# Kernel optimization log

Measured on AMD Instinct MI355X. Metric: run time of the kernel, lower is better.

Reference implementation:

```python
import jax, jax.numpy as jnp
import numpy as np

B, S, E = 1, 2048, 1024
H, KVH = 16, 8
D = E // H            # 64
N_REP = H // KVH      # 2
CLAMP = 50000.0
ROPE_BASE = 10000.0


def setup_inputs() -> dict:
    key = jax.random.key(0)
    ks = jax.random.split(key, 9)
    # RoPE tables: freqs_cis[t, i] = exp(1j * t * base^(-2i/D)), split into cos/sin
    inv_freq = 1.0 / (ROPE_BASE ** (jnp.arange(0, D, 2, dtype=jnp.float32) / D))  # [D/2]
    angles = jnp.arange(S, dtype=jnp.float32)[:, None] * inv_freq[None, :]        # [S, D/2]
    return {
        "x": jax.random.normal(ks[0], (B, S, E), jnp.float32),
        "attn_bias": jax.random.normal(ks[1], (B, H, S, S), jnp.float32) * 0.1,
        "freqs_cos": jnp.cos(angles),
        "freqs_sin": jnp.sin(angles),
        "wq_w": jax.random.normal(ks[2], (E, E), jnp.float32) * (E ** -0.5),
        "wk_w": jax.random.normal(ks[3], (KVH * D, E), jnp.float32) * (E ** -0.5),
        "wk_b": jax.random.normal(ks[4], (KVH * D,), jnp.float32) * 0.01,
        "wv_w": jax.random.normal(ks[5], (KVH * D, E), jnp.float32) * (E ** -0.5),
        "wv_b": jax.random.normal(ks[6], (KVH * D,), jnp.float32) * 0.01,
        "wo_w": jax.random.normal(ks[7], (E, E), jnp.float32) * (E ** -0.5),
        "wo_b": jax.random.normal(ks[8], (E,), jnp.float32) * 0.01,
    }


def _rope(t, cos, sin):
    # t: [b, s, h, d]; pairs (t[..., 2i], t[..., 2i+1]) treated as complex.
    tr = t.reshape(*t.shape[:-1], -1, 2)          # [b, s, h, d/2, 2]
    xr, xi = tr[..., 0], tr[..., 1]
    c = cos[None, :, None, :]                     # [1, s, 1, d/2]
    s = sin[None, :, None, :]
    out = jnp.stack([xr * c - xi * s, xr * s + xi * c], axis=-1)
    return out.reshape(t.shape)


def reference(x, attn_bias, freqs_cos, freqs_sin,
              wq_w, wk_w, wk_b, wv_w, wv_b, wo_w, wo_b):
    bsz, seqlen, _ = x.shape
    xq = (x @ wq_w.T).reshape(bsz, seqlen, H, D)
    xk = (x @ wk_w.T + wk_b).reshape(bsz, seqlen, KVH, D)
    xv = (x @ wv_w.T + wv_b).reshape(bsz, seqlen, KVH, D)
    # inline RoPE on q and k
    xq = _rope(xq, freqs_cos, freqs_sin)
    xk = _rope(xk, freqs_cos, freqs_sin)
    # GQA: repeat kv heads (kv-head h maps to query heads [h*n_rep, (h+1)*n_rep))
    keys = jnp.repeat(xk, N_REP, axis=2)          # [b, s, H, d]
    values = jnp.repeat(xv, N_REP, axis=2)
    # [b, h, q, k] scores with scaling, clamp, bias
    scores = jnp.einsum('bqhd,bkhd->bhqk', xq, keys) / jnp.sqrt(jnp.float32(D))
    scores = jnp.clip(scores, -CLAMP, CLAMP) + attn_bias
    attn_weights = jax.nn.softmax(scores.astype(jnp.float32), axis=-1).astype(xq.dtype)
    out = jnp.einsum('bhqk,bkhd->bqhd', attn_weights, values)
    out = out.reshape(bsz, seqlen, H * D)
    out = out @ wo_w.T + wo_b
    return out, attn_weights
```

## Files before the change

kernel.cpp:

```cpp
#include <hip/hip_runtime.h>
#include <hip/hip_bf16.h>
#include <math.h>

#define SEQ 2048
#define EMB 1024
#define NH 16
#define NKVH 8
#define HD 64

typedef __attribute__((ext_vector_type(8))) short short8;
typedef __attribute__((ext_vector_type(4))) float float4v;

static __device__ __forceinline__ float bf2f(ushort u) {
    union { unsigned int i; float f; } v; v.i = ((unsigned int)u) << 16; return v.f;
}
static __device__ __forceinline__ ushort f2bf(float f) {
    union { float f; unsigned int i; } v; v.f = f;
    unsigned int x = v.i;
    return (ushort)((x + 0x7fffu + ((x >> 16) & 1u)) >> 16);
}
static __device__ __forceinline__ float4v mfma16(short8 a, short8 b, float4v c) {
    return __builtin_amdgcn_mfma_f32_16x16x32_bf16(a, b, c, 0, 0, 0);
}

__global__ void cvt_f32_bf16(const float* __restrict__ src, ushort* __restrict__ dst, int n) {
    int i = blockIdx.x * 256 + threadIdx.x;
    if (i < n) dst[i] = f2bf(src[i]);
}

__global__ __launch_bounds__(256) void gemm_qkv(
    const ushort* __restrict__ x16,
    const ushort* __restrict__ wq16,
    const ushort* __restrict__ wk16,
    const ushort* __restrict__ wv16,
    float* __restrict__ C)
{
    const int l  = threadIdx.x & 63;
    const int w  = threadIdx.x >> 6;
    const int mt = blockIdx.x;
    const int nt = blockIdx.y;
    const int m0  = mt * 64 + (w & 1) * 32;
    const int n0g = nt * 64 + (w >> 1) * 32;
    const ushort* Wp; int nb;
    if (nt < 16)      { Wp = wq16; nb = n0g; }
    else if (nt < 24) { Wp = wk16; nb = n0g - 1024; }
    else              { Wp = wv16; nb = n0g - 1536; }
    const int lr = l & 15, lq = l >> 4;
    float4v acc[2][2] = {};
    const ushort* ap0 = x16 + (m0 + lr) * 1024 + lq * 8;
    const ushort* ap1 = ap0 + 16 * 1024;
    const ushort* bp0 = Wp + (nb + lr) * 1024 + lq * 8;
    const ushort* bp1 = bp0 + 16 * 1024;
    for (int kk = 0; kk < 1024; kk += 32) {
        short8 a0 = *(const short8*)(ap0 + kk);
        short8 a1 = *(const short8*)(ap1 + kk);
        short8 b0 = *(const short8*)(bp0 + kk);
        short8 b1 = *(const short8*)(bp1 + kk);
        acc[0][0] = mfma16(a0, b0, acc[0][0]);
        acc[0][1] = mfma16(a0, b1, acc[0][1]);
        acc[1][0] = mfma16(a1, b0, acc[1][0]);
        acc[1][1] = mfma16(a1, b1, acc[1][1]);
    }
    for (int i = 0; i < 2; i++)
        for (int j = 0; j < 2; j++)
            for (int r = 0; r < 4; r++) {
                int row = m0 + i * 16 + lq * 4 + r;
                int col = nt * 64 + (w >> 1) * 32 + j * 16 + lr;
                C[row * 2048 + col] = acc[i][j][r];
            }
}

__global__ void pack_rope(
    const float* __restrict__ C,
    const float* __restrict__ fcos,
    const float* __restrict__ fsin,
    const float* __restrict__ wk_b,
    const float* __restrict__ wv_b,
    ushort* __restrict__ qh, ushort* __restrict__ ql,
    ushort* __restrict__ kh, ushort* __restrict__ kl,
    ushort* __restrict__ v16)
{
    const int s = blockIdx.x;
    const int t = threadIdx.x;
    const float* Cs = C + s * 2048;
    for (int p = t; p < 512; p += 256) {
        int h = p >> 5, d2 = p & 31;
        float xr = Cs[h * 64 + 2 * d2];
        float xi = Cs[h * 64 + 2 * d2 + 1];
        float c = fcos[s * 32 + d2], sn = fsin[s * 32 + d2];
        float o0 = xr * c - xi * sn;
        float o1 = xr * sn + xi * c;
        int base = (h * 2048 + s) * 64 + 2 * d2;
        ushort h0 = f2bf(o0), h1 = f2bf(o1);
        qh[base] = h0; qh[base + 1] = h1;
        ql[base]     = f2bf(o0 - bf2f(h0));
        ql[base + 1] = f2bf(o1 - bf2f(h1));
    }
    for (int p = t; p < 256; p += 256) {
        int g = p >> 5, d2 = p & 31;
        float xr = Cs[1024 + g * 64 + 2 * d2]     + wk_b[g * 64 + 2 * d2];
        float xi = Cs[1024 + g * 64 + 2 * d2 + 1] + wk_b[g * 64 + 2 * d2 + 1];
        float c = fcos[s * 32 + d2], sn = fsin[s * 32 + d2];
        float o0 = xr * c - xi * sn;
        float o1 = xr * sn + xi * c;
        int base = (g * 2048 + s) * 64 + 2 * d2;
        ushort h0 = f2bf(o0), h1 = f2bf(o1);
        kh[base] = h0; kh[base + 1] = h1;
        kl[base]     = f2bf(o0 - bf2f(h0));
        kl[base + 1] = f2bf(o1 - bf2f(h1));
    }
    for (int i = t; i < 512; i += 256) {
        v16[s * 512 + i] = f2bf(Cs[1536 + i] + wv_b[i]);
    }
}

__global__ void transpose_v(const ushort* __restrict__ v16, ushort* __restrict__ vt) {
    __shared__ ushort tile[64][65];
    const int bx = blockIdx.x;
    const int by = blockIdx.y;
    const int t = threadIdx.x;
    const int tc = t & 63, tr = t >> 6;
    for (int i = 0; i < 64; i += 4)
        tile[tr + i][tc] = v16[(by * 64 + tr + i) * 512 + bx * 64 + tc];
    __syncthreads();
    for (int i = 0; i < 64; i += 4)
        vt[(bx * 64 + tr + i) * 2048 + by * 64 + tc] = tile[tc][tr + i];
}

__global__ __launch_bounds__(256) void attn_kernel(
    const ushort* __restrict__ qh, const ushort* __restrict__ ql,
    const ushort* __restrict__ kh, const ushort* __restrict__ kl,
    const ushort* __restrict__ vt,
    const float* __restrict__ bias,
    float* __restrict__ attn_out,
    ushort* __restrict__ o16,
    float* __restrict__ rowsum_ws)
{
    __shared__ ushort e16[16 * 2048];
    const int blk = blockIdx.x;
    const int h = blk >> 7, qt = blk & 127;
    const int q0 = qt * 16;
    const int g = h >> 1;
    const int t = threadIdx.x, l = t & 63, w = t >> 6;
    const int lr = l & 15, lq = l >> 4;

    const ushort* qb  = qh + (h * 2048 + q0 + lr) * 64 + lq * 8;
    const ushort* qlb = ql + (h * 2048 + q0 + lr) * 64 + lq * 8;
    short8 a_h0 = *(const short8*)(qb);
    short8 a_h1 = *(const short8*)(qb + 32);
    short8 a_l0 = *(const short8*)(qlb);
    short8 a_l1 = *(const short8*)(qlb + 32);

    const float* bias_base = bias + ((size_t)(h * 2048 + q0)) * 2048;

    for (int kt = w * 16; kt < 2048; kt += 64) {
        const ushort* kb  = kh + (g * 2048 + kt + lr) * 64 + lq * 8;
        const ushort* klb = kl + (g * 2048 + kt + lr) * 64 + lq * 8;
        short8 b_h0 = *(const short8*)(kb);
        short8 b_h1 = *(const short8*)(kb + 32);
        short8 b_l0 = *(const short8*)(klb);
        short8 b_l1 = *(const short8*)(klb + 32);
        float4v acc = {};
        acc = mfma16(a_h0, b_h0, acc);
        acc = mfma16(a_h1, b_h1, acc);
        acc = mfma16(a_l0, b_h0, acc);
        acc = mfma16(a_l1, b_h1, acc);
        acc = mfma16(a_h0, b_l0, acc);
        acc = mfma16(a_h1, b_l1, acc);
        for (int r = 0; r < 4; r++) {
            int row = lq * 4 + r;
            int col = kt + lr;
            float sv = acc[r] * 0.125f;
            sv = fminf(fmaxf(sv, -50000.f), 50000.f);
            sv += bias_base[(size_t)row * 2048 + col];
            float e = __expf(sv);
            int sw = ((((col >> 3) ^ (row & 7)) << 3) | (col & 7));
            e16[row * 2048 + sw] = f2bf(e);
        }
    }
    __syncthreads();

    {
        int row = t >> 4, seg = t & 15;
        float rs = 0.f;
        for (int k = 0; k < 128; k++) {
            int col = seg * 128 + k;
            int sw = ((((col >> 3) ^ (row & 7)) << 3) | (col & 7));
            rs += bf2f(e16[row * 2048 + sw]);
        }
        for (int m = 1; m < 16; m <<= 1) rs += __shfl_xor(rs, m, 64);
        if (seg == 0) rowsum_ws[blk * 16 + row] = 1.f / rs;
    }
    __syncthreads();

    {
        float* aout = attn_out + ((size_t)(h * 2048 + q0)) * 2048;
        for (int j = 0; j < 128; j++) {
            int idx = j * 256 + t;
            int row = idx >> 11, col = idx & 2047;
            int sw = ((((col >> 3) ^ (row & 7)) << 3) | (col & 7));
            float invs = rowsum_ws[blk * 16 + row];
            aout[(size_t)row * 2048 + col] = bf2f(e16[row * 2048 + sw]) * invs;
        }
    }

    {
        const int d0 = w * 16;
        const ushort* vb = vt + (g * 64 + d0 + lr) * 2048 + lq * 8;
        float4v acc = {};
        for (int kt = 0; kt < 2048; kt += 32) {
            int blk8 = (kt >> 3) + lq;
            short8 a = *(const short8*)(&e16[lr * 2048 + ((blk8 ^ (lr & 7)) << 3)]);
            short8 b = *(const short8*)(vb + kt);
            acc = mfma16(a, b, acc);
        }
        for (int r = 0; r < 4; r++) {
            int row = lq * 4 + r;
            float invs = rowsum_ws[blk * 16 + row];
            o16[(q0 + row) * 1024 + h * 64 + d0 + lr] = f2bf(acc[r] * invs);
        }
    }
}

__global__ __launch_bounds__(256) void gemm_out(
    const ushort* __restrict__ o16,
    const ushort* __restrict__ wo16,
    const float* __restrict__ wo_b,
    float* __restrict__ out)
{
    const int l  = threadIdx.x & 63;
    const int w  = threadIdx.x >> 6;
    const int mt = blockIdx.x;
    const int nt = blockIdx.y;
    const int m0 = mt * 64 + (w & 1) * 32;
    const int n0 = nt * 64 + (w >> 1) * 32;
    const int lr = l & 15, lq = l >> 4;
    float4v acc[2][2] = {};
    const ushort* ap0 = o16 + (m0 + lr) * 1024 + lq * 8;
    const ushort* ap1 = ap0 + 16 * 1024;
    const ushort* bp0 = wo16 + (n0 + lr) * 1024 + lq * 8;
    const ushort* bp1 = bp0 + 16 * 1024;
    for (int kk = 0; kk < 1024; kk += 32) {
        short8 a0 = *(const short8*)(ap0 + kk);
        short8 a1 = *(const short8*)(ap1 + kk);
        short8 b0 = *(const short8*)(bp0 + kk);
        short8 b1 = *(const short8*)(bp1 + kk);
        acc[0][0] = mfma16(a0, b0, acc[0][0]);
        acc[0][1] = mfma16(a0, b1, acc[0][1]);
        acc[1][0] = mfma16(a1, b0, acc[1][0]);
        acc[1][1] = mfma16(a1, b1, acc[1][1]);
    }
    for (int i = 0; i < 2; i++)
        for (int j = 0; j < 2; j++)
            for (int r = 0; r < 4; r++) {
                int row = m0 + i * 16 + lq * 4 + r;
                int col = n0 + j * 16 + lr;
                out[row * 1024 + col] = acc[i][j][r] + wo_b[col];
            }
}

extern "C" void kernel_launch(void* const* d_in, const int* in_sizes, int n_in,
                              void* d_out, int out_size, void* d_ws, size_t ws_size,
                              hipStream_t stream) {
    const float* x      = (const float*)d_in[0];
    const float* abias  = (const float*)d_in[1];
    const float* fcos   = (const float*)d_in[2];
    const float* fsin   = (const float*)d_in[3];
    const float* wq_w   = (const float*)d_in[4];
    const float* wk_w   = (const float*)d_in[5];
    const float* wk_b   = (const float*)d_in[6];
    const float* wv_w   = (const float*)d_in[7];
    const float* wv_b   = (const float*)d_in[8];
    const float* wo_w   = (const float*)d_in[9];
    const float* wo_b   = (const float*)d_in[10];

    float* out_proj = (float*)d_out;
    float* out_attn = (float*)d_out + (size_t)2048 * 1024;

    char* ws = (char*)d_ws;
    const size_t MB = 1024 * 1024;
    ushort* x16  = (ushort*)(ws + 0 * MB);
    ushort* wq16 = (ushort*)(ws + 4 * MB);
    ushort* wk16 = (ushort*)(ws + 6 * MB);
    ushort* wv16 = (ushort*)(ws + 7 * MB);
    ushort* wo16 = (ushort*)(ws + 8 * MB);
    float*  Cqkv = (float*) (ws + 10 * MB);
    ushort* qh   = (ushort*)(ws + 26 * MB);
    ushort* qlb  = (ushort*)(ws + 30 * MB);
    ushort* kh   = (ushort*)(ws + 34 * MB);
    ushort* klb  = (ushort*)(ws + 36 * MB);
    ushort* v16  = (ushort*)(ws + 38 * MB);
    ushort* vt   = (ushort*)(ws + 40 * MB);
    ushort* o16  = (ushort*)(ws + 42 * MB);
    float*  rsum = (float*) (ws + 46 * MB);

    cvt_f32_bf16<<<(2048 * 1024 + 255) / 256, 256, 0, stream>>>(x, x16, 2048 * 1024);
    cvt_f32_bf16<<<(1024 * 1024 + 255) / 256, 256, 0, stream>>>(wq_w, wq16, 1024 * 1024);
    cvt_f32_bf16<<<(512 * 1024 + 255) / 256, 256, 0, stream>>>(wk_w, wk16, 512 * 1024);
    cvt_f32_bf16<<<(512 * 1024 + 255) / 256, 256, 0, stream>>>(wv_w, wv16, 512 * 1024);
    cvt_f32_bf16<<<(1024 * 1024 + 255) / 256, 256, 0, stream>>>(wo_w, wo16, 1024 * 1024);

    gemm_qkv<<<dim3(32, 32), 256, 0, stream>>>(x16, wq16, wk16, wv16, Cqkv);

    pack_rope<<<2048, 256, 0, stream>>>(Cqkv, fcos, fsin, wk_b, wv_b, qh, qlb, kh, klb, v16);

    transpose_v<<<dim3(8, 32), 256, 0, stream>>>(v16, vt);

    attn_kernel<<<NH * 128, 256, 0, stream>>>(qh, qlb, kh, klb, vt, abias, out_attn, o16, rsum);

    gemm_out<<<dim3(32, 16), 256, 0, stream>>>(o16, wo16, wo_b, out_proj);
}
```

Baseline: 724.6 us.

## Fuse conversions, widen attention blocks, overlap P·V with vectorized attn-weight writes

Merges the five f32-to-bf16 conversion launches into one kernel that converts four elements per thread with vector loads and stores. The attention kernel goes to 512 threads: the score loop is split across 8 waves, the row sums are computed with 16-byte LDS reads and kept in shared memory instead of a global workspace, and waves 4-7 write the normalized attention weights with float4 stores while waves 0-3 run the P·V MFMA. This targets launch overhead, scalar global stores and serialization of the two epilogue phases, at the cost of higher per-block thread count and register pressure.

```diff
diff --git a/kernel.cpp b/kernel.cpp
--- a/kernel.cpp
+++ b/kernel.cpp
@@ -10,6 +10,7 @@
 
 typedef __attribute__((ext_vector_type(8))) short short8;
 typedef __attribute__((ext_vector_type(4))) float float4v;
+typedef __attribute__((ext_vector_type(4))) unsigned short ushort4v;
 
 static __device__ __forceinline__ float bf2f(ushort u) {
     union { unsigned int i; float f; } v; v.i = ((unsigned int)u) << 16; return v.f;
@@ -23,9 +24,24 @@
     return __builtin_amdgcn_mfma_f32_16x16x32_bf16(a, b, c, 0, 0, 0);
 }
 
-__global__ void cvt_f32_bf16(const float* __restrict__ src, ushort* __restrict__ dst, int n) {
+__global__ void cvt_all(const float* __restrict__ x, const float* __restrict__ wq,
+                        const float* __restrict__ wk, const float* __restrict__ wv,
+                        const float* __restrict__ wo,
+                        ushort* __restrict__ x16, ushort* __restrict__ wq16,
+                        ushort* __restrict__ wk16, ushort* __restrict__ wv16,
+                        ushort* __restrict__ wo16)
+{
     int i = blockIdx.x * 256 + threadIdx.x;
-    if (i < n) dst[i] = f2bf(src[i]);
+    const float* s; ushort* d; int off;
+    if (i < 524288)       { s = x;  d = x16;  off = i; }
+    else if (i < 786432)  { s = wq; d = wq16; off = i - 524288; }
+    else if (i < 917504)  { s = wk; d = wk16; off = i - 786432; }
+    else if (i < 1048576) { s = wv; d = wv16; off = i - 917504; }
+    else                  { s = wo; d = wo16; off = i - 1048576; }
+    float4v v = *(const float4v*)(s + (size_t)off * 4);
+    ushort4v u;
+    u.x = f2bf(v.x); u.y = f2bf(v.y); u.z = f2bf(v.z); u.w = f2bf(v.w);
+    *(ushort4v*)(d + (size_t)off * 4) = u;
 }
 
 __global__ __launch_bounds__(256) void gemm_qkv(
@@ -127,16 +143,16 @@
         vt[(bx * 64 + tr + i) * 2048 + by * 64 + tc] = tile[tc][tr + i];
 }
 
-__global__ __launch_bounds__(256) void attn_kernel(
+__global__ __launch_bounds__(512) void attn_kernel(
     const ushort* __restrict__ qh, const ushort* __restrict__ ql,
     const ushort* __restrict__ kh, const ushort* __restrict__ kl,
     const ushort* __restrict__ vt,
     const float* __restrict__ bias,
     float* __restrict__ attn_out,
-    ushort* __restrict__ o16,
-    float* __restrict__ rowsum_ws)
+    ushort* __restrict__ o16)
 {
     __shared__ ushort e16[16 * 2048];
+    __shared__ float invs_s[16];
     const int blk = blockIdx.x;
     const int h = blk >> 7, qt = blk & 127;
     const int q0 = qt * 16;
@@ -153,7 +169,7 @@
 
     const float* bias_base = bias + ((size_t)(h * 2048 + q0)) * 2048;
 
-    for (int kt = w * 16; kt < 2048; kt += 64) {
+    for (int kt = w * 16; kt < 2048; kt += 128) {
         const ushort* kb  = kh + (g * 2048 + kt + lr) * 64 + lq * 8;
         const ushort* klb = kl + (g * 2048 + kt + lr) * 64 + lq * 8;
         short8 b_h0 = *(const short8*)(kb);
@@ -181,30 +197,23 @@
     __syncthreads();
 
     {
-        int row = t >> 4, seg = t & 15;
+        int row = t >> 5, c32 = t & 31;
         float rs = 0.f;
-        for (int k = 0; k < 128; k++) {
-            int col = seg * 128 + k;
-            int sw = ((((col >> 3) ^ (row & 7)) << 3) | (col & 7));
-            rs += bf2f(e16[row * 2048 + sw]);
-        }
-        for (int m = 1; m < 16; m <<= 1) rs += __shfl_xor(rs, m, 64);
-        if (seg == 0) rowsum_ws[blk * 16 + row] = 1.f / rs;
+        for (int j = 0; j < 8; j++) {
+            int cb = c32 * 8 + j;
+            short8 e = *(const short8*)(&e16[row * 2048 + ((cb ^ (row & 7)) << 3)]);
+            for (int u = 0; u < 8; u++) rs += bf2f(e[u]);
+        }
+        rs += __shfl_xor(rs, 1, 64);
+        rs += __shfl_xor(rs, 2, 64);
+        rs += __shfl_xor(rs, 4, 64);
+        rs += __shfl_xor(rs, 8, 64);
+        rs += __shfl_xor(rs, 16, 64);
+        if (c32 == 0) invs_s[row] = 1.f / rs;
     }
     __syncthreads();
 
-    {
-        float* aout = attn_out + ((size_t)(h * 2048 + q0)) * 2048;
-        for (int j = 0; j < 128; j++) {
-            int idx = j * 256 + t;
-            int row = idx >> 11, col = idx & 2047;
-            int sw = ((((col >> 3) ^ (row & 7)) << 3) | (col & 7));
-            float invs = rowsum_ws[blk * 16 + row];
-            aout[(size_t)row * 2048 + col] = bf2f(e16[row * 2048 + sw]) * invs;
-        }
-    }
-
-    {
+    if (w < 4) {
         const int d0 = w * 16;
         const ushort* vb = vt + (g * 64 + d0 + lr) * 2048 + lq * 8;
         float4v acc = {};
@@ -216,8 +225,22 @@
         }
         for (int r = 0; r < 4; r++) {
             int row = lq * 4 + r;
-            float invs = rowsum_ws[blk * 16 + row];
-            o16[(q0 + row) * 1024 + h * 64 + d0 + lr] = f2bf(acc[r] * invs);
+            o16[(q0 + row) * 1024 + h * 64 + d0 + lr] = f2bf(acc[r] * invs_s[row]);
+        }
+    } else {
+        float* aout = attn_out + ((size_t)(h * 2048 + q0)) * 2048;
+        const int t2 = t - 256;
+        for (int row = 0; row < 16; row++) {
+            short8 e = *(const short8*)(&e16[row * 2048 + ((t2 ^ (row & 7)) << 3)]);
+            float invs = invs_s[row];
+            float4v o0, o1;
+            o0.x = bf2f(e[0]) * invs; o0.y = bf2f(e[1]) * invs;
+            o0.z = bf2f(e[2]) * invs; o0.w = bf2f(e[3]) * invs;
+            o1.x = bf2f(e[4]) * invs; o1.y = bf2f(e[5]) * invs;
+            o1.z = bf2f(e[6]) * invs; o1.w = bf2f(e[7]) * invs;
+            float* p = aout + (size_t)row * 2048 + t2 * 8;
+            *(float4v*)(p) = o0;
+            *(float4v*)(p + 4) = o1;
         }
     }
 }
@@ -292,21 +315,12 @@
     ushort* v16  = (ushort*)(ws + 38 * MB);
     ushort* vt   = (ushort*)(ws + 40 * MB);
     ushort* o16  = (ushort*)(ws + 42 * MB);
-    float*  rsum = (float*) (ws + 46 * MB);
-
-    cvt_f32_bf16<<<(2048 * 1024 + 255) / 256, 256, 0, stream>>>(x, x16, 2048 * 1024);
-    cvt_f32_bf16<<<(1024 * 1024 + 255) / 256, 256, 0, stream>>>(wq_w, wq16, 1024 * 1024);
-    cvt_f32_bf16<<<(512 * 1024 + 255) / 256, 256, 0, stream>>>(wk_w, wk16, 512 * 1024);
-    cvt_f32_bf16<<<(512 * 1024 + 255) / 256, 256, 0, stream>>>(wv_w, wv16, 512 * 1024);
-    cvt_f32_bf16<<<(1024 * 1024 + 255) / 256, 256, 0, stream>>>(wo_w, wo16, 1024 * 1024);
-
+
+    cvt_all<<<5120, 256, 0, stream>>>(x, wq_w, wk_w, wv_w, wo_w,
+                                      x16, wq16, wk16, wv16, wo16);
     gemm_qkv<<<dim3(32, 32), 256, 0, stream>>>(x16, wq16, wk16, wv16, Cqkv);
-
     pack_rope<<<2048, 256, 0, stream>>>(Cqkv, fcos, fsin, wk_b, wv_b, qh, qlb, kh, klb, v16);
-
     transpose_v<<<dim3(8, 32), 256, 0, stream>>>(v16, vt);
-
-    attn_kernel<<<NH * 128, 256, 0, stream>>>(qh, qlb, kh, klb, vt, abias, out_attn, o16, rsum);
-
+    attn_kernel<<<NH * 128, 512, 0, stream>>>(qh, qlb, kh, klb, vt, abias, out_attn, o16);
     gemm_out<<<dim3(32, 16), 256, 0, stream>>>(o16, wo16, wo_b, out_proj);
 }
```

Result: no change. 711.5 us (-1.8%).
